# Kernel optimization log

Measured on AMD Instinct MI355X. Metric: run time of the kernel, lower is better.

Reference implementation:

```python
import jax, jax.numpy as jnp
import numpy as np


def conv2d(x, w, b=None, pad=0):
    out = jax.lax.conv_general_dilated(
        x, w, window_strides=(1, 1), padding=[(pad, pad), (pad, pad)],
        dimension_numbers=('NCHW', 'OIHW', 'NCHW'))
    if b is not None:
        out = out + b[None, :, None, None]
    return out


def maxpool2(x):
    return jax.lax.reduce_window(x, -jnp.inf, jax.lax.max,
                                 (1, 1, 2, 2), (1, 1, 2, 2), 'VALID')


def conv_offset_2d(x, offset_w):
    """ConvOffset2D: learn per-pixel (dy,dx) offsets via a 3x3 conv (C->2C, no
    bias), then bilinearly resample x at grid+offset. Faithful to the repo,
    including its raw (B,2C,H,W)->(B*C,H,W,2) memory reinterpretation."""
    B, C, H, W = x.shape
    off = conv2d(x, offset_w, pad=1)                  # (B, 2C, H, W)
    off = off.reshape(B * C, H, W, 2)                 # raw row-major reshape (as in repo)
    xf = x.reshape(B * C, H, W)
    gy, gx = jnp.meshgrid(jnp.arange(H, dtype=x.dtype),
                          jnp.arange(W, dtype=x.dtype), indexing='ij')
    coords = off + jnp.stack([gy, gx], axis=-1)       # (BC, H, W, 2) = (y, x)
    cy = jnp.clip(coords[..., 0], 0.0, float(H - 1))
    cx = jnp.clip(coords[..., 1], 0.0, float(W - 1))
    y0 = jnp.floor(cy)
    x0 = jnp.floor(cx)
    y0i = y0.astype(jnp.int32)
    x0i = x0.astype(jnp.int32)
    y1i = jnp.ceil(cy).astype(jnp.int32)
    x1i = jnp.ceil(cx).astype(jnp.int32)
    bidx = jnp.arange(B * C)[:, None, None]
    v_lt = xf[bidx, y0i, x0i]
    v_rt = xf[bidx, y0i, x1i]
    v_lb = xf[bidx, y1i, x0i]
    v_rb = xf[bidx, y1i, x1i]
    tx = cx - x0
    ty = cy - y0
    v_t = v_lt + (v_rt - v_lt) * tx
    v_b = v_lb + (v_rb - v_lb) * tx
    out = v_t + (v_b - v_t) * ty
    return out.reshape(B, C, H, W)


def setup_inputs() -> dict:
    key = jax.random.key(0)
    ks = jax.random.split(key, 9)
    B = 2048
    inp = {
        'x': jax.random.normal(ks[0], (B, 1, 28, 28), dtype=jnp.float32),
        'off1_w': jax.random.normal(ks[1], (2, 1, 3, 3), dtype=jnp.float32) * 0.01,
        'conv1_w': jax.random.normal(ks[2], (16, 1, 5, 5), dtype=jnp.float32) * 0.1,
        'conv1_b': jax.random.normal(ks[3], (16,), dtype=jnp.float32) * 0.01,
        'off2_w': jax.random.normal(ks[4], (32, 16, 3, 3), dtype=jnp.float32) * 0.01,
        'conv2_w': jax.random.normal(ks[5], (32, 16, 5, 5), dtype=jnp.float32) * 0.05,
        'conv2_b': jax.random.normal(ks[6], (32,), dtype=jnp.float32) * 0.01,
        'fc_w': jax.random.normal(ks[7], (10, 32 * 7 * 7), dtype=jnp.float32) * 0.02,
        'fc_b': jax.random.normal(ks[8], (10,), dtype=jnp.float32) * 0.01,
    }
    return inp


def reference(x, off1_w, conv1_w, conv1_b, off2_w, conv2_w, conv2_b, fc_w, fc_b):
    # block 1: deform sample -> 5x5 conv pad 2 -> relu -> maxpool 2
    h = conv_offset_2d(x, off1_w)
    h = maxpool2(jax.nn.relu(conv2d(h, conv1_w, conv1_b, pad=2)))   # (B,16,14,14)
    # block 2
    h = conv_offset_2d(h, off2_w)
    h = maxpool2(jax.nn.relu(conv2d(h, conv2_w, conv2_b, pad=2)))   # (B,32,7,7)
    # classifier
    flat = h.reshape(h.shape[0], -1)                                # (B, 1568)
    return flat @ fc_w.T + fc_b
```

## Files before the change

### kernel.cpp

```cpp
#include <hip/hip_runtime.h>
#include <hip/hip_bf16.h>


#define B_IMG 2048

typedef short bf16x8 __attribute__((ext_vector_type(8)));
typedef float f32x4 __attribute__((ext_vector_type(4)));

__global__ __launch_bounds__(256) void k_prep(const float* __restrict__ w_off2,
                                              const float* __restrict__ w_c2,
                                              const float* __restrict__ w_c1,
                                              __hip_bfloat16* __restrict__ wqo,
                                              __hip_bfloat16* __restrict__ wq2,
                                              __hip_bfloat16* __restrict__ wqc1) {
    int e = blockIdx.x * 256 + threadIdx.x;
    if (e < 5120) {
        int sp = e >> 10, rem = e & 1023, oc = rem >> 5, k = rem & 31;
        int sl = k >> 4, ic = k & 15, s = 2 * sp + sl;
        wqo[e] = __float2bfloat16(s < 9 ? w_off2[(oc * 16 + ic) * 9 + s] : 0.f);
    } else if (e < 18432) {
        int e2 = e - 5120;
        int sp = e2 >> 10, rem = e2 & 1023, oc = rem >> 5, k = rem & 31;
        int sl = k >> 4, ic = k & 15, s = 2 * sp + sl;
        wq2[e2] = __float2bfloat16(s < 25 ? w_c2[(oc * 16 + ic) * 25 + s] : 0.f);
    } else if (e < 18944) {
        int e3 = e - 18432;
        int oc = e3 >> 5, k = e3 & 31;
        wqc1[e3] = __float2bfloat16(k < 25 ? w_c1[oc * 25 + k] : 0.f);
    }
}

__global__ __launch_bounds__(256, 4) void k_net(const float* __restrict__ x,
                                                const float* __restrict__ off1_w,
                                                const __hip_bfloat16* __restrict__ wqc1,
                                                const float* __restrict__ conv1_b,
                                                const __hip_bfloat16* __restrict__ wqo,
                                                const __hip_bfloat16* __restrict__ wq2,
                                                const float* __restrict__ conv2_b,
                                                const float* __restrict__ fc_w,
                                                const float* __restrict__ fc_b,
                                                float* __restrict__ out) {
    __shared__ __align__(16) char s5[12544];
    __shared__ __align__(16) __hip_bfloat16 imgb[16 * 16 * 16];
    __shared__ __align__(16) __hip_bfloat16 img2b[18 * 20 * 16];

    float* xs = (float*)s5;
    __hip_bfloat16* img2bf = (__hip_bfloat16*)(s5 + 3600);
    _Float16* offbuf = (_Float16*)s5;
    float* pl    = (float*)s5;
    float* wredp = (float*)(s5 + 6272);

    int b = blockIdx.x, t = threadIdx.x;

    for (int i = t; i < 900; i += 256) xs[i] = 0.f;
    for (int i = t; i < 576; i += 256) ((unsigned int*)img2bf)[i] = 0u;
    for (int i = t; i < 2048; i += 256) ((unsigned int*)imgb)[i] = 0u;
    for (int i = t; i < 2880; i += 256) ((unsigned int*)img2b)[i] = 0u;
    __syncthreads();
    for (int i = t; i < 784; i += 256)
        xs[(i / 28 + 1) * 30 + (i % 28) + 1] = x[b * 784 + i];
    __syncthreads();

    for (int p = t; p < 784; p += 256) {
        int h = p / 28, w = p % 28;
        float off[2];
        int flat0 = h * 56 + w * 2;
#pragma unroll
        for (int k = 0; k < 2; ++k) {
            int flat = flat0 + k;
            int c = flat / 784;
            int r = flat % 784;
            int hh = r / 28, ww = r % 28;
            float s = 0.f;
#pragma unroll
            for (int dy = 0; dy < 3; ++dy)
#pragma unroll
                for (int dx = 0; dx < 3; ++dx)
                    s += off1_w[c * 9 + dy * 3 + dx] * xs[(hh + dy) * 30 + ww + dx];
            off[k] = s;
        }
        float cy = fminf(fmaxf((float)h + off[0], 0.f), 27.f);
        float cx = fminf(fmaxf((float)w + off[1], 0.f), 27.f);
        float y0f = floorf(cy), x0f = floorf(cx);
        int y0 = (int)y0f, x0 = (int)x0f;
        int y1 = (int)ceilf(cy), x1 = (int)ceilf(cx);
        float ty = cy - y0f, tx = cx - x0f;
        float vlt = xs[(y0 + 1) * 30 + x0 + 1], vrt = xs[(y0 + 1) * 30 + x1 + 1];
        float vlb = xs[(y1 + 1) * 30 + x0 + 1], vrb = xs[(y1 + 1) * 30 + x1 + 1];
        float vt = vlt + (vrt - vlt) * tx;
        float vb = vlb + (vrb - vlb) * tx;
        img2bf[(h + 2) * 36 + (w + 2)] = __float2bfloat16(vt + (vb - vt) * ty);
    }
    __syncthreads();

    int wv_ = t >> 6, li = t & 63;
    int lx = li & 15, lg = li >> 4;

    {
        const bf16x8* wc1v = (const bf16x8*)wqc1;
        bf16x8 af1 = wc1v[lx * 4 + lg];
        float b4[4];
#pragma unroll
        for (int r = 0; r < 4; ++r) b4[r] = conv1_b[lg * 4 + r];
        int toff[8];
        unsigned short msk[8];
#pragma unroll
        for (int j = 0; j < 8; ++j) {
            int tt = 8 * lg + j;
            int dyq = tt / 5, dxq = tt - 5 * dyq;
            toff[j] = (tt < 25) ? (dyq * 36 + dxq) : 0;
            msk[j] = (tt < 25) ? 0xFFFFu : 0u;
        }
        int ypstart = (wv_ < 2) ? wv_ * 4 : 8 + (wv_ - 2) * 3;
        int ypcnt = (wv_ < 2) ? 4 : 3;
        const unsigned short* ib28 = (const unsigned short*)img2bf;
        for (int u = 0; u < 4; ++u) {
            if (u < ypcnt) {
                int yp = ypstart + u;
#pragma unroll
                for (int xh = 0; xh < 2; ++xh) {
                    int xp = xh * 16 + lx;
                    f32x4 a0 = (f32x4){0.f, 0.f, 0.f, 0.f};
                    f32x4 a1 = (f32x4){0.f, 0.f, 0.f, 0.f};
#pragma unroll
                    for (int yy = 0; yy < 2; ++yy) {
                        int base16 = (2 * yp + yy) * 36 + xp;
                        unsigned short uu[8];
#pragma unroll
                        for (int j = 0; j < 8; ++j)
                            uu[j] = (unsigned short)(ib28[base16 + toff[j]] & msk[j]);
                        bf16x8 bq = {(short)uu[0], (short)uu[1], (short)uu[2], (short)uu[3],
                                     (short)uu[4], (short)uu[5], (short)uu[6], (short)uu[7]};
                        if (yy == 0)
                            a0 = __builtin_amdgcn_mfma_f32_16x16x32_bf16(af1, bq, a0, 0, 0, 0);
                        else
                            a1 = __builtin_amdgcn_mfma_f32_16x16x32_bf16(af1, bq, a1, 0, 0, 0);
                    }
#pragma unroll
                    for (int r = 0; r < 4; ++r) {
                        float v = fmaxf(fmaxf(a0[r], a1[r]) + b4[r], 0.f);
                        float p = __shfl_xor(v, 1);
                        float m = fmaxf(v, p);
                        if (((xp & 1) == 0) && xp < 28) {
                            int oc = lg * 4 + r;
                            imgb[(yp + 1) * 256 + ((xp >> 1) + 1) * 16 + oc] = __float2bfloat16(m);
                        }
                    }
                }
            }
        }
    }
    __syncthreads();

    int och = wv_ & 1, yh = wv_ >> 1;
    int nrows = yh ? 6 : 8;

    {
        const bf16x8* wA = (const bf16x8*)wqo;
        bf16x8 afA[5];
#pragma unroll
        for (int sp = 0; sp < 5; ++sp)
            afA[sp] = wA[(sp * 32 + och * 16 + lx) * 4 + lg];
        int slA = lg >> 1, icsel = lg & 1;
        f32x4 acc[8];
#pragma unroll
        for (int y = 0; y < 8; ++y) acc[y] = (f32x4){0.f, 0.f, 0.f, 0.f};
        const bf16x8* ib = (const bf16x8*)imgb;
#pragma unroll
        for (int sp = 0; sp < 5; ++sp) {
            int s0 = 2 * sp + slA;
            int dy = s0 / 3, dx = s0 % 3;
            if (s0 >= 9) { dy = 0; dx = 0; }
            int base = dy * 32 + (lx + dx) * 2 + icsel;
#pragma unroll
            for (int y = 0; y < 8; ++y) {
                if (y < nrows) {
                    bf16x8 bfr = ib[base + (yh * 8 + y) * 32];
                    acc[y] = __builtin_amdgcn_mfma_f32_16x16x32_bf16(afA[sp], bfr, acc[y], 0, 0, 0);
                }
            }
        }
        if (lx < 14) {
#pragma unroll
            for (int y = 0; y < 8; ++y) {
                if (y < nrows) {
                    int yy = yh * 8 + y;
#pragma unroll
                    for (int r = 0; r < 4; ++r) {
                        int oc = och * 16 + lg * 4 + r;
                        offbuf[oc * 196 + yy * 14 + lx] = (_Float16)acc[y][r];
                    }
                }
            }
        }
    }
    __syncthreads();

    for (int o = t; o < 3136; o += 256) {
        int c = o & 15, rem = o >> 4;
        int h = rem / 14, w = rem % 14;
        int pidx = c * 196 + h * 14 + w;
        unsigned int pr = ((const unsigned int*)offbuf)[pidx];
        unsigned short lo16 = (unsigned short)(pr & 0xFFFFu);
        unsigned short hi16 = (unsigned short)(pr >> 16);
        float offy = (float)(*(const _Float16*)&lo16);
        float offx = (float)(*(const _Float16*)&hi16);
        float cy = fminf(fmaxf((float)h + offy, 0.f), 13.f);
        float cx = fminf(fmaxf((float)w + offx, 0.f), 13.f);
        float y0f = floorf(cy), x0f = floorf(cx);
        int y0 = (int)y0f, x0 = (int)x0f;
        int y1 = (int)ceilf(cy), x1 = (int)ceilf(cx);
        float ty = cy - y0f, tx = cx - x0f;
        float vlt = __bfloat162float(imgb[(y0 + 1) * 256 + (x0 + 1) * 16 + c]);
        float vrt = __bfloat162float(imgb[(y0 + 1) * 256 + (x1 + 1) * 16 + c]);
        float vlb = __bfloat162float(imgb[(y1 + 1) * 256 + (x0 + 1) * 16 + c]);
        float vrb = __bfloat162float(imgb[(y1 + 1) * 256 + (x1 + 1) * 16 + c]);
        float vt = vlt + (vrt - vlt) * tx;
        float vb = vlb + (vrb - vlb) * tx;
        img2b[((h + 2) * 20 + (w + 2)) * 16 + c] = __float2bfloat16(vt + (vb - vt) * ty);
    }
    __syncthreads();

    {
        const bf16x8* wB = (const bf16x8*)wq2;
        bf16x8 af[13];
#pragma unroll
        for (int sp = 0; sp < 13; ++sp)
            af[sp] = wB[(sp * 32 + och * 16 + lx) * 4 + lg];
        int sl = lg >> 1, icg = lg & 1;
        float bias_r[4];
#pragma unroll
        for (int r = 0; r < 4; ++r) bias_r[r] = conv2_b[och * 16 + lg * 4 + r];
        f32x4 acc[8];
#pragma unroll
        for (int y = 0; y < 8; ++y) acc[y] = (f32x4){0.f, 0.f, 0.f, 0.f};
        const bf16x8* ib2 = (const bf16x8*)img2b;
#pragma unroll
        for (int sp = 0; sp < 13; ++sp) {
            int s0 = 2 * sp + sl;
            int dy = s0 / 5, dx = s0 % 5;
            if (s0 >= 25) { dy = 0; dx = 0; }
            int base = (lx + dx) * 2 + icg;
#pragma unroll
            for (int y = 0; y < 8; ++y) {
                if (y < nrows) {
                    bf16x8 bfr = ib2[base + (yh * 8 + y + dy) * 40];
                    acc[y] = __builtin_amdgcn_mfma_f32_16x16x32_bf16(af[sp], bfr, acc[y], 0, 0, 0);
                }
            }
        }
        __syncthreads();
        int npool = yh ? 3 : 4;
#pragma unroll
        for (int u = 0; u < 4; ++u) {
            if (u < npool) {
                int i = yh * 4 + u;
#pragma unroll
                for (int r = 0; r < 4; ++r) {
                    int oc = och * 16 + lg * 4 + r;
                    float v = fmaxf(fmaxf(acc[2 * u][r], acc[2 * u + 1][r]) + bias_r[r], 0.f);
                    float p = __shfl_xor(v, 1);
                    float m = fmaxf(v, p);
                    if (((lx & 1) == 0) && lx < 14)
                        pl[oc * 49 + i * 7 + (lx >> 1)] = m;
                }
            }
        }
    }
    __syncthreads();

    float facc[10];
#pragma unroll
    for (int o = 0; o < 10; ++o) facc[o] = 0.f;
#pragma unroll
    for (int it = 0; it < 2; ++it) {
        int k = t * 4 + it * 1024;
        if (k < 1568) {
            float4 v = *(const float4*)&pl[k];
#pragma unroll
            for (int o = 0; o < 10; ++o) {
                float4 w4 = *(const float4*)&fc_w[o * 1568 + k];
                facc[o] += v.x * w4.x + v.y * w4.y + v.z * w4.z + v.w * w4.w;
            }
        }
    }
#pragma unroll
    for (int o = 0; o < 10; ++o) {
        float s = facc[o];
#pragma unroll
        for (int m = 32; m > 0; m >>= 1) s += __shfl_xor(s, m);
        if (li == 0) wredp[o * 4 + wv_] = s;
    }
    __syncthreads();
    if (t < 10)
        out[b * 10 + t] = fc_b[t] + wredp[t * 4] + wredp[t * 4 + 1] + wredp[t * 4 + 2] + wredp[t * 4 + 3];
}

extern "C" void kernel_launch(void* const* d_in, const int* in_sizes, int n_in,
                              void* d_out, int out_size, void* d_ws, size_t ws_size,
                              hipStream_t stream) {
    const float* x       = (const float*)d_in[0];
    const float* off1_w  = (const float*)d_in[1];
    const float* conv1_w = (const float*)d_in[2];
    const float* conv1_b = (const float*)d_in[3];
    const float* off2_w  = (const float*)d_in[4];
    const float* conv2_w = (const float*)d_in[5];
    const float* conv2_b = (const float*)d_in[6];
    const float* fc_w    = (const float*)d_in[7];
    const float* fc_b    = (const float*)d_in[8];
    float* out = (float*)d_out;

    char* ws = (char*)d_ws;
    __hip_bfloat16* wqo  = (__hip_bfloat16*)ws;
    __hip_bfloat16* wq2  = (__hip_bfloat16*)(ws + 10240);
    __hip_bfloat16* wqc1 = (__hip_bfloat16*)(ws + 36864);

    k_prep<<<74, 256, 0, stream>>>(off2_w, conv2_w, conv1_w, wqo, wq2, wqc1);
    k_net<<<B_IMG, 256, 0, stream>>>(x, off1_w, wqc1, conv1_b, wqo, wq2,
                                     conv2_b, fc_w, fc_b, out);
}
```

Baseline: 60.52 us.

## Alias conv2 input buffer onto scratch LDS to cut shared memory footprint

Removes the dedicated img2b LDS array (about 11.5 KB) and places it in the s5 scratch region. The deformable samples are held in registers until a barrier, then written over the offset buffer. The pooled output and reduction buffers move into imgb, which lets one barrier after the conv2 MFMA loop be dropped. Lower LDS per block may allow more resident blocks per CU, at the cost of higher register pressure from the 13 buffered sample values.

Measured after the change: 61.63 us. Within noise of the previous version (+1.8%).

```diff
diff --git a/kernel.cpp b/kernel.cpp
--- a/kernel.cpp
+++ b/kernel.cpp
@@ -42,20 +42,19 @@
                                                 float* __restrict__ out) {
     __shared__ __align__(16) char s5[12544];
     __shared__ __align__(16) __hip_bfloat16 imgb[16 * 16 * 16];
-    __shared__ __align__(16) __hip_bfloat16 img2b[18 * 20 * 16];
 
     float* xs = (float*)s5;
     __hip_bfloat16* img2bf = (__hip_bfloat16*)(s5 + 3600);
     _Float16* offbuf = (_Float16*)s5;
-    float* pl    = (float*)s5;
-    float* wredp = (float*)(s5 + 6272);
+    __hip_bfloat16* img2b = (__hip_bfloat16*)s5;
+    float* pl    = (float*)imgb;
+    float* wredp = (float*)((char*)imgb + 6272);
 
     int b = blockIdx.x, t = threadIdx.x;
 
     for (int i = t; i < 900; i += 256) xs[i] = 0.f;
     for (int i = t; i < 576; i += 256) ((unsigned int*)img2bf)[i] = 0u;
     for (int i = t; i < 2048; i += 256) ((unsigned int*)imgb)[i] = 0u;
-    for (int i = t; i < 2880; i += 256) ((unsigned int*)img2b)[i] = 0u;
     __syncthreads();
     for (int i = t; i < 784; i += 256)
         xs[(i / 28 + 1) * 30 + (i % 28) + 1] = x[b * 784 + i];
@@ -196,28 +195,53 @@
     }
     __syncthreads();
 
-    for (int o = t; o < 3136; o += 256) {
-        int c = o & 15, rem = o >> 4;
-        int h = rem / 14, w = rem % 14;
-        int pidx = c * 196 + h * 14 + w;
-        unsigned int pr = ((const unsigned int*)offbuf)[pidx];
-        unsigned short lo16 = (unsigned short)(pr & 0xFFFFu);
-        unsigned short hi16 = (unsigned short)(pr >> 16);
-        float offy = (float)(*(const _Float16*)&lo16);
-        float offx = (float)(*(const _Float16*)&hi16);
-        float cy = fminf(fmaxf((float)h + offy, 0.f), 13.f);
-        float cx = fminf(fmaxf((float)w + offx, 0.f), 13.f);
-        float y0f = floorf(cy), x0f = floorf(cx);
-        int y0 = (int)y0f, x0 = (int)x0f;
-        int y1 = (int)ceilf(cy), x1 = (int)ceilf(cx);
-        float ty = cy - y0f, tx = cx - x0f;
-        float vlt = __bfloat162float(imgb[(y0 + 1) * 256 + (x0 + 1) * 16 + c]);
-        float vrt = __bfloat162float(imgb[(y0 + 1) * 256 + (x1 + 1) * 16 + c]);
-        float vlb = __bfloat162float(imgb[(y1 + 1) * 256 + (x0 + 1) * 16 + c]);
-        float vrb = __bfloat162float(imgb[(y1 + 1) * 256 + (x1 + 1) * 16 + c]);
-        float vt = vlt + (vrt - vlt) * tx;
-        float vb = vlb + (vrb - vlb) * tx;
-        img2b[((h + 2) * 20 + (w + 2)) * 16 + c] = __float2bfloat16(vt + (vb - vt) * ty);
+    {
+        float vres[13];
+#pragma unroll
+        for (int u = 0; u < 13; ++u) {
+            int o = t + u * 256;
+            if (o < 3136) {
+                int c = o & 15, rem = o >> 4;
+                int h = rem / 14, w = rem % 14;
+                int pidx = c * 196 + h * 14 + w;
+                unsigned int pr = ((const unsigned int*)offbuf)[pidx];
+                unsigned short lo16 = (unsigned short)(pr & 0xFFFFu);
+                unsigned short hi16 = (unsigned short)(pr >> 16);
+                float offy = (float)(*(const _Float16*)&lo16);
+                float offx = (float)(*(const _Float16*)&hi16);
+                float cy = fminf(fmaxf((float)h + offy, 0.f), 13.f);
+                float cx = fminf(fmaxf((float)w + offx, 0.f), 13.f);
+                float y0f = floorf(cy), x0f = floorf(cx);
+                int y0 = (int)y0f, x0 = (int)x0f;
+                int y1 = (int)ceilf(cy), x1 = (int)ceilf(cx);
+                float ty = cy - y0f, tx = cx - x0f;
+                float vlt = __bfloat162float(imgb[(y0 + 1) * 256 + (x0 + 1) * 16 + c]);
+                float vrt = __bfloat162float(imgb[(y0 + 1) * 256 + (x1 + 1) * 16 + c]);
+                float vlb = __bfloat162float(imgb[(y1 + 1) * 256 + (x0 + 1) * 16 + c]);
+                float vrb = __bfloat162float(imgb[(y1 + 1) * 256 + (x1 + 1) * 16 + c]);
+                float vt = vlt + (vrt - vlt) * tx;
+                float vb = vlb + (vrb - vlb) * tx;
+                vres[u] = vt + (vb - vt) * ty;
+            }
+        }
+        __syncthreads();
+        for (int p = t; p < 360; p += 256) {
+            int r = p / 20, cc = p % 20;
+            if (r < 2 || r > 15 || cc < 2 || cc > 15) {
+                unsigned int* dst = (unsigned int*)&img2b[p * 16];
+#pragma unroll
+                for (int q = 0; q < 8; ++q) dst[q] = 0u;
+            }
+        }
+#pragma unroll
+        for (int u = 0; u < 13; ++u) {
+            int o = t + u * 256;
+            if (o < 3136) {
+                int c = o & 15, rem = o >> 4;
+                int h = rem / 14, w = rem % 14;
+                img2b[((h + 2) * 20 + (w + 2)) * 16 + c] = __float2bfloat16(vres[u]);
+            }
+        }
     }
     __syncthreads();
 
@@ -249,7 +273,6 @@
                 }
             }
         }
-        __syncthreads();
         int npool = yh ? 3 : 4;
 #pragma unroll
         for (int u = 0; u < 4; ++u) {
```
